# Optimization experiments

Hardware: AMD Instinct MI355X
Metric: run time of the kernel (lower is better)

Reference implementation:

```python
import jax, jax.numpy as jnp
import numpy as np

INV_SQRT2 = 0.7071067811865476
SCALES = 3


def dwt_analysis(x, dec_lo, dec_hi, scales):
    """Multi-level 1D DWT along last axis (pywt/ptwt convention).
    x: [B, D]. dec_lo/dec_hi are cross-correlation filters (torch conv1d
    semantics, i.e. the flipped pywt decomposition filters as stored by the
    repo). Returns [cA_s | cD_s | ... | cD_1] truncated to the last D columns
    (identity for Haar on power-of-two D)."""
    flen = dec_lo.shape[0]
    pad = (2 * flen - 3) // 2  # ptwt zero-pad; 0 for Haar (flen=2)
    filt = jnp.stack([dec_lo, dec_hi])[:, None, :]  # [2, 1, flen]
    lo = x[:, None, :]  # [B, 1, D]
    highs = []
    for _ in range(scales):
        out = jax.lax.conv_general_dilated(
            lo, filt, window_strides=(2,), padding=[(pad, pad)],
            dimension_numbers=('NCH', 'OIH', 'NCH'))  # [B, 2, D/2]
        lo = out[:, 0:1, :]
        highs.append(out[:, 1, :])
    coeffs = jnp.concatenate([lo[:, 0, :]] + highs[::-1], axis=-1)
    return coeffs[:, -x.shape[-1]:]


def setup_inputs() -> dict:
    key = jax.random.key(0)
    k1, k2, k3, k4, k5 = jax.random.split(key, 5)
    B, D = 4096, 4096
    x = jax.random.normal(k1, (B, D), jnp.float32)
    diag_s = jax.random.normal(k2, (D,), jnp.float32)
    diag_g = jax.random.normal(k3, (D,), jnp.float32)
    diag_b = jax.random.normal(k4, (D,), jnp.float32)
    perm = jax.random.permutation(k5, jnp.arange(D))  # random column permutation
    # Haar analysis filters in cross-correlation (torch conv1d) orientation
    dec_lo = jnp.array([INV_SQRT2, INV_SQRT2], jnp.float32)
    dec_hi = jnp.array([INV_SQRT2, -INV_SQRT2], jnp.float32)
    return {"x": x, "diag_s": diag_s, "diag_g": diag_g, "diag_b": diag_b,
            "dec_lo": dec_lo, "dec_hi": dec_hi, "perm": perm, "scales": SCALES}


def reference(x, diag_s, diag_g, diag_b, dec_lo, dec_hi, perm, scales):
    # mul_b: x @ diag(b) == columnwise scale (same math, no O(d^2) matmul)
    h = x * diag_b
    h = dwt_analysis(h, dec_lo, dec_hi, scales)
    # mul_p: x @ P for a permutation matrix == column gather
    h = jnp.take(h, perm, axis=1)
    h = h * diag_g  # mul_g
    h = dwt_analysis(h, dec_lo, dec_hi, scales)
    return h * diag_s  # mul_s
```

## Files before the change

kernel.cpp:

```cpp
#include <hip/hip_runtime.h>


#define D   4096
#define NT  256

#define C_INV_SQRT2 0.70710678118654752440f

static __device__ __forceinline__ int swz(int i) {
    return i ^ ((i >> 5) & 31);
}

static __device__ __forceinline__ void dwt3_reg(const float v[16],
                                                float a3[2], float d3[2],
                                                float d2[4], float d1[8]) {
    float a1[8];
    #pragma unroll
    for (int j = 0; j < 8; ++j) {
        a1[j] = (v[2 * j] + v[2 * j + 1]) * C_INV_SQRT2;
        d1[j] = (v[2 * j] - v[2 * j + 1]) * C_INV_SQRT2;
    }
    float a2[4];
    #pragma unroll
    for (int j = 0; j < 4; ++j) {
        a2[j] = (a1[2 * j] + a1[2 * j + 1]) * C_INV_SQRT2;
        d2[j] = (a1[2 * j] - a1[2 * j + 1]) * C_INV_SQRT2;
    }
    #pragma unroll
    for (int j = 0; j < 2; ++j) {
        a3[j] = (a2[2 * j] + a2[2 * j + 1]) * C_INV_SQRT2;
        d3[j] = (a2[2 * j] - a2[2 * j + 1]) * C_INV_SQRT2;
    }
}

__global__ __launch_bounds__(NT) void wavelet_row_kernel(
    const float* __restrict__ x,
    const float* __restrict__ diag_s,
    const float* __restrict__ diag_g,
    const float* __restrict__ diag_b,
    const int*   __restrict__ perm,
    float*       __restrict__ out)
{
    __shared__ float buf[D];

    const int t = threadIdx.x;
    const size_t row = blockIdx.x;

    float v[16];
    {
        const float4* x4 = (const float4*)(x + row * (size_t)D);
        const float4* b4 = (const float4*)diag_b;
        #pragma unroll
        for (int k = 0; k < 4; ++k) {
            float4 xv = x4[4 * t + k];
            float4 bv = b4[4 * t + k];
            v[4 * k + 0] = xv.x * bv.x;
            v[4 * k + 1] = xv.y * bv.y;
            v[4 * k + 2] = xv.z * bv.z;
            v[4 * k + 3] = xv.w * bv.w;
        }
    }

    float a3[2], d3[2], d2[4], d1[8];
    dwt3_reg(v, a3, d3, d2, d1);

    #pragma unroll
    for (int j = 0; j < 2; ++j) buf[swz(2 * t + j)]        = a3[j];
    #pragma unroll
    for (int j = 0; j < 2; ++j) buf[swz(512 + 2 * t + j)]  = d3[j];
    #pragma unroll
    for (int j = 0; j < 4; ++j) buf[swz(1024 + 4 * t + j)] = d2[j];
    #pragma unroll
    for (int j = 0; j < 8; ++j) buf[swz(2048 + 8 * t + j)] = d1[j];

    __syncthreads();

    float w[16];
    {
        const int4*   p4 = (const int4*)perm;
        const float4* g4 = (const float4*)diag_g;
        int pidx[16];
        #pragma unroll
        for (int k = 0; k < 4; ++k) {
            int4 pv = p4[4 * t + k];
            pidx[4 * k + 0] = pv.x;
            pidx[4 * k + 1] = pv.y;
            pidx[4 * k + 2] = pv.z;
            pidx[4 * k + 3] = pv.w;
        }
        #pragma unroll
        for (int k = 0; k < 4; ++k) {
            float4 gv = g4[4 * t + k];
            w[4 * k + 0] = buf[swz(pidx[4 * k + 0])] * gv.x;
            w[4 * k + 1] = buf[swz(pidx[4 * k + 1])] * gv.y;
            w[4 * k + 2] = buf[swz(pidx[4 * k + 2])] * gv.z;
            w[4 * k + 3] = buf[swz(pidx[4 * k + 3])] * gv.w;
        }
    }

    float b3[2], e3[2], e2[4], e1[8];
    dwt3_reg(w, b3, e3, e2, e1);

    float* orow = out + row * (size_t)D;
    {
        const float2* s2 = (const float2*)diag_s;
        float2* o2 = (float2*)orow;
        float2 sv, ov;
        sv = s2[t];
        ov.x = b3[0] * sv.x; ov.y = b3[1] * sv.y;
        o2[t] = ov;
        sv = s2[256 + t];
        ov.x = e3[0] * sv.x; ov.y = e3[1] * sv.y;
        o2[256 + t] = ov;
    }
    {
        const float4* s4 = (const float4*)diag_s;
        float4* o4 = (float4*)orow;
        float4 sv = s4[256 + t];
        float4 ov;
        ov.x = e2[0] * sv.x; ov.y = e2[1] * sv.y;
        ov.z = e2[2] * sv.z; ov.w = e2[3] * sv.w;
        o4[256 + t] = ov;
        #pragma unroll
        for (int k = 0; k < 2; ++k) {
            float4 sw = s4[512 + 2 * t + k];
            float4 ow;
            ow.x = e1[4 * k + 0] * sw.x; ow.y = e1[4 * k + 1] * sw.y;
            ow.z = e1[4 * k + 2] * sw.z; ow.w = e1[4 * k + 3] * sw.w;
            o4[512 + 2 * t + k] = ow;
        }
    }
}

extern "C" void kernel_launch(void* const* d_in, const int* in_sizes, int n_in,
                              void* d_out, int out_size, void* d_ws, size_t ws_size,
                              hipStream_t stream) {
    const float* x      = (const float*)d_in[0];
    const float* diag_s = (const float*)d_in[1];
    const float* diag_g = (const float*)d_in[2];
    const float* diag_b = (const float*)d_in[3];
    const int* perm     = (const int*)d_in[6];
    float* out          = (float*)d_out;

    const int B = 4096;
    wavelet_row_kernel<<<B, NT, 0, stream>>>(x, diag_s, diag_g, diag_b, perm, out);
}
```

Measured before the change: 139.9 us.

## Process four rows per block, reuse diag/perm registers, nontemporal stores

```diff
diff --git a/kernel.cpp b/kernel.cpp
--- a/kernel.cpp
+++ b/kernel.cpp
@@ -3,8 +3,12 @@
 
 #define D   4096
 #define NT  256
+#define R   4
 
 #define C_INV_SQRT2 0.70710678118654752440f
+
+typedef float vf2 __attribute__((ext_vector_type(2)));
+typedef float vf4 __attribute__((ext_vector_type(4)));
 
 static __device__ __forceinline__ int swz(int i) {
     return i ^ ((i >> 5) & 31);
@@ -32,7 +36,7 @@
     }
 }
 
-__global__ __launch_bounds__(NT) void wavelet_row_kernel(
+__global__ __launch_bounds__(NT) void wavelet_rows_kernel(
     const float* __restrict__ x,
     const float* __restrict__ diag_s,
     const float* __restrict__ diag_g,
@@ -40,93 +44,99 @@
     const int*   __restrict__ perm,
     float*       __restrict__ out)
 {
-    __shared__ float buf[D];
+    __shared__ float buf[2][D];
 
     const int t = threadIdx.x;
-    const size_t row = blockIdx.x;
+    const size_t row0 = (size_t)blockIdx.x * R;
 
-    float v[16];
+    float db[16], dg[16];
+    int   pidx[16];
     {
-        const float4* x4 = (const float4*)(x + row * (size_t)D);
-        const float4* b4 = (const float4*)diag_b;
+        const vf4* b4 = (const vf4*)diag_b;
+        const vf4* g4 = (const vf4*)diag_g;
+        const int4* p4 = (const int4*)perm;
         #pragma unroll
         for (int k = 0; k < 4; ++k) {
-            float4 xv = x4[4 * t + k];
-            float4 bv = b4[4 * t + k];
-            v[4 * k + 0] = xv.x * bv.x;
-            v[4 * k + 1] = xv.y * bv.y;
-            v[4 * k + 2] = xv.z * bv.z;
-            v[4 * k + 3] = xv.w * bv.w;
+            vf4 bv = b4[4 * t + k];
+            db[4 * k + 0] = bv.x; db[4 * k + 1] = bv.y;
+            db[4 * k + 2] = bv.z; db[4 * k + 3] = bv.w;
+            vf4 gv = g4[4 * t + k];
+            dg[4 * k + 0] = gv.x; dg[4 * k + 1] = gv.y;
+            dg[4 * k + 2] = gv.z; dg[4 * k + 3] = gv.w;
+            int4 pv = p4[4 * t + k];
+            pidx[4 * k + 0] = pv.x; pidx[4 * k + 1] = pv.y;
+            pidx[4 * k + 2] = pv.z; pidx[4 * k + 3] = pv.w;
         }
     }
+    vf2 sA, sD3;
+    vf4 sD2, sD1a, sD1b;
+    {
+        const vf2* s2 = (const vf2*)diag_s;
+        const vf4* s4 = (const vf4*)diag_s;
+        sA   = s2[t];
+        sD3  = s2[256 + t];
+        sD2  = s4[256 + t];
+        sD1a = s4[512 + 2 * t];
+        sD1b = s4[512 + 2 * t + 1];
+    }
 
-    float a3[2], d3[2], d2[4], d1[8];
-    dwt3_reg(v, a3, d3, d2, d1);
+    for (int r = 0; r < R; ++r) {
+        float* b = buf[r & 1];
+        const vf4* x4 = (const vf4*)(x + (row0 + r) * (size_t)D);
 
-    #pragma unroll
-    for (int j = 0; j < 2; ++j) buf[swz(2 * t + j)]        = a3[j];
-    #pragma unroll
-    for (int j = 0; j < 2; ++j) buf[swz(512 + 2 * t + j)]  = d3[j];
-    #pragma unroll
-    for (int j = 0; j < 4; ++j) buf[swz(1024 + 4 * t + j)] = d2[j];
-    #pragma unroll
-    for (int j = 0; j < 8; ++j) buf[swz(2048 + 8 * t + j)] = d1[j];
-
-    __syncthreads();
-
-    float w[16];
-    {
-        const int4*   p4 = (const int4*)perm;
-        const float4* g4 = (const float4*)diag_g;
-        int pidx[16];
+        float v[16];
         #pragma unroll
         for (int k = 0; k < 4; ++k) {
-            int4 pv = p4[4 * t + k];
-            pidx[4 * k + 0] = pv.x;
-            pidx[4 * k + 1] = pv.y;
-            pidx[4 * k + 2] = pv.z;
-            pidx[4 * k + 3] = pv.w;
+            vf4 xv = x4[4 * t + k];
+            v[4 * k + 0] = xv.x * db[4 * k + 0];
+            v[4 * k + 1] = xv.y * db[4 * k + 1];
+            v[4 * k + 2] = xv.z * db[4 * k + 2];
+            v[4 * k + 3] = xv.w * db[4 * k + 3];
         }
+
+        float a3[2], d3[2], d2[4], d1[8];
+        dwt3_reg(v, a3, d3, d2, d1);
+
         #pragma unroll
-        for (int k = 0; k < 4; ++k) {
-            float4 gv = g4[4 * t + k];
-            w[4 * k + 0] = buf[swz(pidx[4 * k + 0])] * gv.x;
-            w[4 * k + 1] = buf[swz(pidx[4 * k + 1])] * gv.y;
-            w[4 * k + 2] = buf[swz(pidx[4 * k + 2])] * gv.z;
-            w[4 * k + 3] = buf[swz(pidx[4 * k + 3])] * gv.w;
+        for (int j = 0; j < 2; ++j) b[swz(2 * t + j)]        = a3[j];
+        #pragma unroll
+        for (int j = 0; j < 2; ++j) b[swz(512 + 2 * t + j)]  = d3[j];
+        #pragma unroll
+        for (int j = 0; j < 4; ++j) b[swz(1024 + 4 * t + j)] = d2[j];
+        #pragma unroll
+        for (int j = 0; j < 8; ++j) b[swz(2048 + 8 * t + j)] = d1[j];
+
+        __syncthreads();
+
+        float w[16];
+        #pragma unroll
+        for (int k = 0; k < 16; ++k) {
+            w[k] = b[swz(pidx[k])] * dg[k];
         }
-    }
 
-    float b3[2], e3[2], e2[4], e1[8];
-    dwt3_reg(w, b3, e3, e2, e1);
+        float b3[2], e3[2], e2[4], e1[8];
+        dwt3_reg(w, b3, e3, e2, e1);
 
-    float* orow = out + row * (size_t)D;
-    {
-        const float2* s2 = (const float2*)diag_s;
-        float2* o2 = (float2*)orow;
-        float2 sv, ov;
-        sv = s2[t];
-        ov.x = b3[0] * sv.x; ov.y = b3[1] * sv.y;
-        o2[t] = ov;
-        sv = s2[256 + t];
-        ov.x = e3[0] * sv.x; ov.y = e3[1] * sv.y;
-        o2[256 + t] = ov;
-    }
-    {
-        const float4* s4 = (const float4*)diag_s;
-        float4* o4 = (float4*)orow;
-        float4 sv = s4[256 + t];
-        float4 ov;
-        ov.x = e2[0] * sv.x; ov.y = e2[1] * sv.y;
-        ov.z = e2[2] * sv.z; ov.w = e2[3] * sv.w;
-        o4[256 + t] = ov;
-        #pragma unroll
-        for (int k = 0; k < 2; ++k) {
-            float4 sw = s4[512 + 2 * t + k];
-            float4 ow;
-            ow.x = e1[4 * k + 0] * sw.x; ow.y = e1[4 * k + 1] * sw.y;
-            ow.z = e1[4 * k + 2] * sw.z; ow.w = e1[4 * k + 3] * sw.w;
-            o4[512 + 2 * t + k] = ow;
+        float* orow = out + (row0 + r) * (size_t)D;
+        {
+            vf2* o2 = (vf2*)orow;
+            vf2 ov;
+            ov.x = b3[0] * sA.x;  ov.y = b3[1] * sA.y;
+            __builtin_nontemporal_store(ov, &o2[t]);
+            ov.x = e3[0] * sD3.x; ov.y = e3[1] * sD3.y;
+            __builtin_nontemporal_store(ov, &o2[256 + t]);
+
+            vf4* o4 = (vf4*)orow;
+            vf4 o;
+            o.x = e2[0] * sD2.x; o.y = e2[1] * sD2.y;
+            o.z = e2[2] * sD2.z; o.w = e2[3] * sD2.w;
+            __builtin_nontemporal_store(o, &o4[256 + t]);
+            o.x = e1[0] * sD1a.x; o.y = e1[1] * sD1a.y;
+            o.z = e1[2] * sD1a.z; o.w = e1[3] * sD1a.w;
+            __builtin_nontemporal_store(o, &o4[512 + 2 * t]);
+            o.x = e1[4] * sD1b.x; o.y = e1[5] * sD1b.y;
+            o.z = e1[6] * sD1b.z; o.w = e1[7] * sD1b.w;
+            __builtin_nontemporal_store(o, &o4[512 + 2 * t + 1]);
         }
     }
 }
@@ -141,6 +151,6 @@
     const int* perm     = (const int*)d_in[6];
     float* out          = (float*)d_out;
 
-    const int B = 4096;
-    wavelet_row_kernel<<<B, NT, 0, stream>>>(x, diag_s, diag_g, diag_b, perm, out);
+    const int B = 4096 / R;
+    wavelet_rows_kernel<<<B, NT, 0, stream>>>(x, diag_s, diag_g, diag_b, perm, out);
 }
```

Result: faster. 129.3 us (-7.6%).
